# Optimization experiments

Hardware: AMD Instinct MI355X
Metric: run time of the kernel (lower is better)

## Reference

```python
import jax, jax.numpy as jnp
import numpy as np

S, B, D_IN = 2048, 32, 512
H, PROJ, L = 1024, 512, 2
LN_EPS = 1e-5


def setup_inputs() -> dict:
    key = jax.random.key(0)
    ks = jax.random.split(key, 4)
    X = jax.random.normal(ks[0], (S, B, D_IN), dtype=jnp.float32)
    W = jax.random.normal(ks[1], (L, 3 * H, D_IN), dtype=jnp.float32) * (1.0 / np.sqrt(D_IN))
    b = jax.random.normal(ks[2], (L, 3 * H), dtype=jnp.float32) * 0.01
    P = jax.random.normal(ks[3], (L, PROJ, H), dtype=jnp.float32) * (1.0 / np.sqrt(H))
    gamma = jnp.ones((L, PROJ), dtype=jnp.float32)
    beta = jnp.zeros((L, PROJ), dtype=jnp.float32)
    return {"X": X, "W": W, "b": b, "P": P, "gamma": gamma, "beta": beta}


def _forget_mult(F, Z):
    # h_t = f_t * z_t + (1 - f_t) * h_{t-1}, h_0 = 0  (ForgetMult, hidden=None)
    def step(c, fz):
        f, z = fz
        c = f * z + (1.0 - f) * c
        return c, c
    c0 = jnp.zeros_like(Z[0])
    _, C = jax.lax.scan(step, c0, (F, Z))
    return C  # (S, B, H)


def _layer_norm(x, g, be):
    mu = jnp.mean(x, axis=-1, keepdims=True)
    var = jnp.mean(jnp.square(x - mu), axis=-1, keepdims=True)
    return (x - mu) * jax.lax.rsqrt(var + LN_EPS) * g + be


def reference(X, W, b, P, gamma, beta):
    inp = X
    last_states = []
    for i in range(L):
        # linear: (S,B,in) @ (in,3H) + b  -> gates
        Y = jnp.einsum('sbd,gd->sbg', inp, W[i]) + b[i]
        Z, F, O = jnp.split(Y, 3, axis=-1)
        Z = jnp.tanh(Z)
        F = jax.nn.sigmoid(F)
        C = _forget_mult(F, Z)                      # (S,B,H)
        Hout = jax.nn.sigmoid(O) * C                # output gate (QRNN-fo)
        inp = jnp.einsum('sbh,ph->sbp', Hout, P[i])  # projection, no bias
        inp = _layer_norm(inp, gamma[i], beta[i])
        last_states.append(C[-1])                   # (B,H)
    next_hidden = jnp.stack(last_states, axis=0)     # (L,B,H)
    return inp, next_hidden
```

## Files before the change

### kernel.cpp

```cpp
#include <hip/hip_runtime.h>
#include <hip/hip_bf16.h>

typedef _Float16 f16x8 __attribute__((ext_vector_type(8)));
typedef _Float16 f16x4 __attribute__((ext_vector_type(4)));
typedef float f32x4 __attribute__((ext_vector_type(4)));

#define SEQ 2048
#define BATCH 32
#define DIN 512
#define HID 1024
#define PROJ 512
#define ROWS (SEQ*BATCH)
#define G3H (3*HID)

#define AS1(p) ((const __attribute__((address_space(1))) void*)(p))
#define AS3(p) ((__attribute__((address_space(3))) void*)(p))

__global__ __launch_bounds__(256)
void cvt_f32_f16(const float* __restrict__ in, _Float16* __restrict__ out, int n4)
{
    int i = blockIdx.x * 256 + threadIdx.x;
    if (i >= n4) return;
    float4 v = ((const float4*)in)[i];
    f16x4 o;
    o[0] = (_Float16)v.x; o[1] = (_Float16)v.y;
    o[2] = (_Float16)v.z; o[3] = (_Float16)v.w;
    ((f16x4*)out)[i] = o;
}

template<int MODE>
__global__ __launch_bounds__(256)
void gemm_lds(const _Float16* __restrict__ A, const _Float16* __restrict__ Bm,
              const float* __restrict__ bias, _Float16* __restrict__ C,
              int N, int K, int HH)
{
    __shared__ __align__(16) _Float16 sA[128][32];
    __shared__ __align__(16) _Float16 sB[128][32];

    const int tid  = threadIdx.x;
    const int lane = tid & 63;
    const int wave = tid >> 6;
    const int wm = wave >> 1;
    const int wn = wave & 1;
    const size_t row0 = (size_t)blockIdx.y * 128;
    const size_t col0 = (size_t)blockIdx.x * 128;

    const int crow = lane >> 2;
    const int ccol = (lane & 3) * 8;

    f32x4 acc[4][4] = {};

    const int rl = lane & 15;
    const int kb = (lane >> 4) * 8;

    const int nk = K / 32;
    for (int kt = 0; kt < nk; ++kt) {
#pragma unroll
        for (int c2 = 0; c2 < 2; ++c2) {
            const int c = wave * 2 + c2;
            const _Float16* ga = A  + (row0 + c * 16 + crow) * (size_t)K + kt * 32 + ccol;
            const _Float16* gb = Bm + (col0 + c * 16 + crow) * (size_t)K + kt * 32 + ccol;
            __builtin_amdgcn_global_load_lds(AS1(ga), AS3(&sA[c * 16][0]), 16, 0, 0);
            __builtin_amdgcn_global_load_lds(AS1(gb), AS3(&sB[c * 16][0]), 16, 0, 0);
        }
        __syncthreads();

        f16x8 af[4], bf[4];
#pragma unroll
        for (int m = 0; m < 4; ++m)
            af[m] = *(const f16x8*)&sA[wm * 64 + m * 16 + rl][kb];
#pragma unroll
        for (int n = 0; n < 4; ++n)
            bf[n] = *(const f16x8*)&sB[wn * 64 + n * 16 + rl][kb];
#pragma unroll
        for (int m = 0; m < 4; ++m)
#pragma unroll
            for (int n = 0; n < 4; ++n)
                acc[m][n] = __builtin_amdgcn_mfma_f32_16x16x32_f16(af[m], bf[n], acc[m][n], 0, 0, 0);
        __syncthreads();
    }

#pragma unroll
    for (int m = 0; m < 4; ++m) {
#pragma unroll
        for (int n = 0; n < 4; ++n) {
            const size_t col = col0 + wn * 64 + n * 16 + rl;
            const size_t row = row0 + wm * 64 + m * 16 + (lane >> 4) * 4;
            float bv = (MODE == 0) ? bias[col] : 0.f;
#pragma unroll
            for (int j = 0; j < 4; ++j) {
                float v = acc[m][n][j];
                if (MODE == 0) {
                    v += bv;
                    if ((int)col < HH) {
                        float vc = fminf(fmaxf(v, -15.f), 15.f);
                        float e = __expf(2.f * vc);
                        v = (e - 1.f) / (e + 1.f);
                    } else {
                        v = 1.f / (1.f + __expf(-v));
                    }
                }
                C[(row + j) * (size_t)N + col] = (_Float16)v;
            }
        }
    }
}

__global__ __launch_bounds__(64)
void scan_kernel(const _Float16* __restrict__ Y, _Float16* __restrict__ Ho,
                 float* __restrict__ carry, float* __restrict__ hid,
                 int nS, int first)
{
    const int t = blockIdx.x * 64 + threadIdx.x;
    const int h = t & (HID - 1);
    const int b = t >> 10;
    const _Float16* pz = Y + (size_t)b * G3H + h;
    _Float16* po = Ho + (size_t)b * HID + h;
    const size_t strideY = (size_t)BATCH * G3H;
    const size_t strideH = (size_t)BATCH * HID;
    float c = first ? 0.f : carry[t];
#pragma unroll 8
    for (int s = 0; s < nS; ++s) {
        float z = (float)pz[(size_t)s * strideY];
        float f = (float)pz[(size_t)s * strideY + HID];
        float o = (float)pz[(size_t)s * strideY + 2 * HID];
        c = f * z + (1.f - f) * c;
        po[(size_t)s * strideH] = (_Float16)(o * c);
    }
    carry[t] = c;
    if (hid) hid[t] = c;
}

template<int OUT32>
__global__ __launch_bounds__(256)
void ln_kernel(const _Float16* __restrict__ Xin, const float* __restrict__ g,
               const float* __restrict__ be, _Float16* __restrict__ o16,
               float* __restrict__ o32)
{
    const int row  = blockIdx.x * 4 + (threadIdx.x >> 6);
    const int lane = threadIdx.x & 63;
    const _Float16* p = Xin + (size_t)row * PROJ + lane * 8;
    f16x8 v = *(const f16x8*)p;
    float x[8];
    float s = 0.f;
#pragma unroll
    for (int j = 0; j < 8; ++j) { x[j] = (float)v[j]; s += x[j]; }
#pragma unroll
    for (int d = 1; d < 64; d <<= 1) s += __shfl_xor(s, d);
    const float mu = s * (1.f / PROJ);
    float s2 = 0.f;
#pragma unroll
    for (int j = 0; j < 8; ++j) { float dd = x[j] - mu; s2 += dd * dd; }
#pragma unroll
    for (int d = 1; d < 64; d <<= 1) s2 += __shfl_xor(s2, d);
    const float rstd = rsqrtf(s2 * (1.f / PROJ) + 1e-5f);

    float y[8];
#pragma unroll
    for (int j = 0; j < 8; ++j)
        y[j] = (x[j] - mu) * rstd * g[lane * 8 + j] + be[lane * 8 + j];

    if (OUT32) {
        float* q = o32 + (size_t)row * PROJ + lane * 8;
        ((float4*)q)[0] = make_float4(y[0], y[1], y[2], y[3]);
        ((float4*)q)[1] = make_float4(y[4], y[5], y[6], y[7]);
    } else {
        f16x8 o;
#pragma unroll
        for (int j = 0; j < 8; ++j) o[j] = (_Float16)y[j];
        *(f16x8*)(o16 + (size_t)row * PROJ + lane * 8) = o;
    }
}

extern "C" void kernel_launch(void* const* d_in, const int* in_sizes, int n_in,
                              void* d_out, int out_size, void* d_ws, size_t ws_size,
                              hipStream_t stream)
{
    const float* X     = (const float*)d_in[0];
    const float* W     = (const float*)d_in[1];
    const float* b     = (const float*)d_in[2];
    const float* P     = (const float*)d_in[3];
    const float* gamma = (const float*)d_in[4];
    const float* beta  = (const float*)d_in[5];
    float* out = (float*)d_out;

    char* w = (char*)d_ws;
    _Float16* Xh = (_Float16*)w; w += (size_t)ROWS * DIN * 2;
    _Float16* Wh = (_Float16*)w; w += (size_t)2 * G3H * DIN * 2;
    _Float16* Ph = (_Float16*)w; w += (size_t)2 * PROJ * HID * 2;
    float* carry = (float*)w;    w += (size_t)BATCH * HID * 4;
    const size_t fixed = (size_t)(w - (char*)d_ws);

    const int cands[7] = {2048, 1024, 512, 256, 128, 64, 32};
    int CS = 32;
    for (int i = 0; i < 7; ++i) {
        size_t need = fixed + (size_t)cands[i] * 32 * (G3H + HID + PROJ) * 2;
        if (need <= ws_size) { CS = cands[i]; break; }
    }
    _Float16* Yg = (_Float16*)w; w += (size_t)CS * 32 * G3H * 2;
    _Float16* Ho = (_Float16*)w; w += (size_t)CS * 32 * HID * 2;
    _Float16* G2 = (_Float16*)w;

    cvt_f32_f16<<<(ROWS * DIN / 4 + 255) / 256, 256, 0, stream>>>(X, Xh, ROWS * DIN / 4);
    cvt_f32_f16<<<(2 * G3H * DIN / 4 + 255) / 256, 256, 0, stream>>>(W, Wh, 2 * G3H * DIN / 4);
    cvt_f32_f16<<<(2 * PROJ * HID / 4 + 255) / 256, 256, 0, stream>>>(P, Ph, 2 * PROJ * HID / 4);

    float* hid = out + (size_t)ROWS * PROJ;
    const int nch = SEQ / CS;
    const int rows = CS * BATCH;

    for (int i = 0; i < 2; ++i) {
        for (int ch = 0; ch < nch; ++ch) {
            const size_t r0 = (size_t)ch * rows;
            gemm_lds<0><<<dim3(G3H / 128, rows / 128), 256, 0, stream>>>(
                Xh + r0 * DIN, Wh + (size_t)i * G3H * DIN, b + i * G3H, Yg, G3H, DIN, HID);
            scan_kernel<<<(BATCH * HID) / 64, 64, 0, stream>>>(
                Yg, Ho, carry, (ch == nch - 1) ? hid + (size_t)i * BATCH * HID : nullptr,
                CS, ch == 0);
            gemm_lds<1><<<dim3(PROJ / 128, rows / 128), 256, 0, stream>>>(
                Ho, Ph + (size_t)i * PROJ * HID, nullptr, G2, PROJ, HID, 0);
            if (i == 0)
                ln_kernel<0><<<rows / 4, 256, 0, stream>>>(G2, gamma, beta, Xh + r0 * PROJ, nullptr);
            else
                ln_kernel<1><<<rows / 4, 256, 0, stream>>>(G2, gamma + PROJ, beta + PROJ, nullptr, out + r0 * PROJ);
        }
    }
}
```

Before: 1.857 ms.

## Parallelize forget-mult scan over sequence segments and double-buffer GEMM LDS tiles

Replaces the single sequential scan over each chunk with a three-pass segmented scan: each of 16 segments computes its affine (A,B) composition, a middle pass chains segment carries, and a second pass recomputes outputs from the segment start states. This multiplies the number of threads working on the recurrence so the latency-bound scan can fill the GPU, at the cost of reading the Z/F gates twice and extra workspace. The GEMM also gains a two-stage LDS buffer that prefetches the next K tile while computing the current one, and uses fast division in the activation epilogue.

Result: faster. 1.590 ms (-14.4%).

```diff
diff --git a/kernel.cpp b/kernel.cpp
--- a/kernel.cpp
+++ b/kernel.cpp
@@ -12,6 +12,8 @@
 #define PROJ 512
 #define ROWS (SEQ*BATCH)
 #define G3H (3*HID)
+#define NSEG 16
+#define NCHAIN (BATCH*HID)
 
 #define AS1(p) ((const __attribute__((address_space(1))) void*)(p))
 #define AS3(p) ((__attribute__((address_space(3))) void*)(p))
@@ -34,8 +36,8 @@
               const float* __restrict__ bias, _Float16* __restrict__ C,
               int N, int K, int HH)
 {
-    __shared__ __align__(16) _Float16 sA[128][32];
-    __shared__ __align__(16) _Float16 sB[128][32];
+    __shared__ __align__(16) _Float16 sA[2][128][32];
+    __shared__ __align__(16) _Float16 sB[2][128][32];
 
     const int tid  = threadIdx.x;
     const int lane = tid & 63;
@@ -52,33 +54,48 @@
 
     const int rl = lane & 15;
     const int kb = (lane >> 4) * 8;
-
     const int nk = K / 32;
+
+    const int c0 = wave * 2, c1 = wave * 2 + 1;
+    const _Float16* gA0 = A  + (row0 + c0 * 16 + crow) * (size_t)K + ccol;
+    const _Float16* gA1 = A  + (row0 + c1 * 16 + crow) * (size_t)K + ccol;
+    const _Float16* gB0 = Bm + (col0 + c0 * 16 + crow) * (size_t)K + ccol;
+    const _Float16* gB1 = Bm + (col0 + c1 * 16 + crow) * (size_t)K + ccol;
+
+#define STAGE(buf, kt)                                                          \
+    do {                                                                        \
+        __builtin_amdgcn_global_load_lds(AS1(gA0 + (size_t)(kt) * 32),          \
+                                         AS3(&sA[buf][c0 * 16][0]), 16, 0, 0);  \
+        __builtin_amdgcn_global_load_lds(AS1(gB0 + (size_t)(kt) * 32),          \
+                                         AS3(&sB[buf][c0 * 16][0]), 16, 0, 0);  \
+        __builtin_amdgcn_global_load_lds(AS1(gA1 + (size_t)(kt) * 32),          \
+                                         AS3(&sA[buf][c1 * 16][0]), 16, 0, 0);  \
+        __builtin_amdgcn_global_load_lds(AS1(gB1 + (size_t)(kt) * 32),          \
+                                         AS3(&sB[buf][c1 * 16][0]), 16, 0, 0);  \
+    } while (0)
+
+    int cur = 0;
+    STAGE(0, 0);
+    __syncthreads();
+
     for (int kt = 0; kt < nk; ++kt) {
-#pragma unroll
-        for (int c2 = 0; c2 < 2; ++c2) {
-            const int c = wave * 2 + c2;
-            const _Float16* ga = A  + (row0 + c * 16 + crow) * (size_t)K + kt * 32 + ccol;
-            const _Float16* gb = Bm + (col0 + c * 16 + crow) * (size_t)K + kt * 32 + ccol;
-            __builtin_amdgcn_global_load_lds(AS1(ga), AS3(&sA[c * 16][0]), 16, 0, 0);
-            __builtin_amdgcn_global_load_lds(AS1(gb), AS3(&sB[c * 16][0]), 16, 0, 0);
-        }
-        __syncthreads();
-
+        if (kt + 1 < nk) STAGE(cur ^ 1, kt + 1);
         f16x8 af[4], bf[4];
 #pragma unroll
         for (int m = 0; m < 4; ++m)
-            af[m] = *(const f16x8*)&sA[wm * 64 + m * 16 + rl][kb];
+            af[m] = *(const f16x8*)&sA[cur][wm * 64 + m * 16 + rl][kb];
 #pragma unroll
         for (int n = 0; n < 4; ++n)
-            bf[n] = *(const f16x8*)&sB[wn * 64 + n * 16 + rl][kb];
+            bf[n] = *(const f16x8*)&sB[cur][wn * 64 + n * 16 + rl][kb];
 #pragma unroll
         for (int m = 0; m < 4; ++m)
 #pragma unroll
             for (int n = 0; n < 4; ++n)
                 acc[m][n] = __builtin_amdgcn_mfma_f32_16x16x32_f16(af[m], bf[n], acc[m][n], 0, 0, 0);
         __syncthreads();
-    }
+        cur ^= 1;
+    }
+#undef STAGE
 
 #pragma unroll
     for (int m = 0; m < 4; ++m) {
@@ -95,9 +112,9 @@
                     if ((int)col < HH) {
                         float vc = fminf(fmaxf(v, -15.f), 15.f);
                         float e = __expf(2.f * vc);
-                        v = (e - 1.f) / (e + 1.f);
+                        v = __fdividef(e - 1.f, e + 1.f);
                     } else {
-                        v = 1.f / (1.f + __expf(-v));
+                        v = __fdividef(1.f, 1.f + __expf(-v));
                     }
                 }
                 C[(row + j) * (size_t)N + col] = (_Float16)v;
@@ -106,29 +123,69 @@
     }
 }
 
-__global__ __launch_bounds__(64)
-void scan_kernel(const _Float16* __restrict__ Y, _Float16* __restrict__ Ho,
-                 float* __restrict__ carry, float* __restrict__ hid,
-                 int nS, int first)
-{
-    const int t = blockIdx.x * 64 + threadIdx.x;
+
+__global__ __launch_bounds__(256)
+void scan_p1(const _Float16* __restrict__ Y, float* __restrict__ Aseg,
+             float* __restrict__ Bseg, int SL)
+{
+    const int t = blockIdx.x * 256 + threadIdx.x;
+    const int g = blockIdx.y;
     const int h = t & (HID - 1);
     const int b = t >> 10;
-    const _Float16* pz = Y + (size_t)b * G3H + h;
-    _Float16* po = Ho + (size_t)b * HID + h;
+    const _Float16* pz = Y + ((size_t)(g * SL) * BATCH + b) * G3H + h;
+    const size_t strideY = (size_t)BATCH * G3H;
+    float A = 1.f, Bv = 0.f;
+#pragma unroll 4
+    for (int k = 0; k < SL; ++k) {
+        float z = (float)pz[0];
+        float f = (float)pz[HID];
+        Bv = f * z + (1.f - f) * Bv;
+        A *= (1.f - f);
+        pz += strideY;
+    }
+    Aseg[(size_t)g * NCHAIN + t] = A;
+    Bseg[(size_t)g * NCHAIN + t] = Bv;
+}
+
+__global__ __launch_bounds__(256)
+void scan_mid(const float* __restrict__ Aseg, const float* __restrict__ Bseg,
+              float* __restrict__ cst, float* __restrict__ carry,
+              float* __restrict__ hid, int first)
+{
+    const int t = blockIdx.x * 256 + threadIdx.x;
+    float c = first ? 0.f : carry[t];
+#pragma unroll
+    for (int g = 0; g < NSEG; ++g) {
+        cst[(size_t)g * NCHAIN + t] = c;
+        c = Bseg[(size_t)g * NCHAIN + t] + Aseg[(size_t)g * NCHAIN + t] * c;
+    }
+    carry[t] = c;
+    if (hid) hid[t] = c;
+}
+
+__global__ __launch_bounds__(256)
+void scan_p2(const _Float16* __restrict__ Y, const float* __restrict__ cst,
+             _Float16* __restrict__ Ho, int SL)
+{
+    const int t = blockIdx.x * 256 + threadIdx.x;
+    const int g = blockIdx.y;
+    const int h = t & (HID - 1);
+    const int b = t >> 10;
+    const _Float16* pz = Y + ((size_t)(g * SL) * BATCH + b) * G3H + h;
+    _Float16* po = Ho + ((size_t)(g * SL) * BATCH + b) * HID + h;
     const size_t strideY = (size_t)BATCH * G3H;
     const size_t strideH = (size_t)BATCH * HID;
-    float c = first ? 0.f : carry[t];
-#pragma unroll 8
-    for (int s = 0; s < nS; ++s) {
-        float z = (float)pz[(size_t)s * strideY];
-        float f = (float)pz[(size_t)s * strideY + HID];
-        float o = (float)pz[(size_t)s * strideY + 2 * HID];
+    float c = cst[(size_t)g * NCHAIN + t];
+#pragma unroll 4
+    for (int k = 0; k < SL; ++k) {
+        float z = (float)pz[0];
+        float f = (float)pz[HID];
+        float o = (float)pz[2 * HID];
         c = f * z + (1.f - f) * c;
-        po[(size_t)s * strideH] = (_Float16)(o * c);
-    }
-    carry[t] = c;
-    if (hid) hid[t] = c;
+        *po = (_Float16)(o * c);
+        pz += strideY;
+        po += strideH;
+    }
 }
 
 template<int OUT32>
@@ -188,7 +245,10 @@
     _Float16* Xh = (_Float16*)w; w += (size_t)ROWS * DIN * 2;
     _Float16* Wh = (_Float16*)w; w += (size_t)2 * G3H * DIN * 2;
     _Float16* Ph = (_Float16*)w; w += (size_t)2 * PROJ * HID * 2;
-    float* carry = (float*)w;    w += (size_t)BATCH * HID * 4;
+    float* carry = (float*)w;    w += (size_t)NCHAIN * 4;
+    float* Aseg  = (float*)w;    w += (size_t)NSEG * NCHAIN * 4;
+    float* Bseg  = (float*)w;    w += (size_t)NSEG * NCHAIN * 4;
+    float* cst   = (float*)w;    w += (size_t)NSEG * NCHAIN * 4;
     const size_t fixed = (size_t)(w - (char*)d_ws);
 
     const int cands[7] = {2048, 1024, 512, 256, 128, 64, 32};
@@ -208,15 +268,18 @@
     float* hid = out + (size_t)ROWS * PROJ;
     const int nch = SEQ / CS;
     const int rows = CS * BATCH;
+    const int SL = CS / NSEG;
 
     for (int i = 0; i < 2; ++i) {
         for (int ch = 0; ch < nch; ++ch) {
             const size_t r0 = (size_t)ch * rows;
             gemm_lds<0><<<dim3(G3H / 128, rows / 128), 256, 0, stream>>>(
                 Xh + r0 * DIN, Wh + (size_t)i * G3H * DIN, b + i * G3H, Yg, G3H, DIN, HID);
-            scan_kernel<<<(BATCH * HID) / 64, 64, 0, stream>>>(
-                Yg, Ho, carry, (ch == nch - 1) ? hid + (size_t)i * BATCH * HID : nullptr,
-                CS, ch == 0);
+            scan_p1<<<dim3(NCHAIN / 256, NSEG), 256, 0, stream>>>(Yg, Aseg, Bseg, SL);
+            scan_mid<<<NCHAIN / 256, 256, 0, stream>>>(
+                Aseg, Bseg, cst, carry,
+                (ch == nch - 1) ? hid + (size_t)i * NCHAIN : nullptr, ch == 0);
+            scan_p2<<<dim3(NCHAIN / 256, NSEG), 256, 0, stream>>>(Yg, cst, Ho, SL);
             gemm_lds<1><<<dim3(PROJ / 128, rows / 128), 256, 0, stream>>>(
                 Ho, Ph + (size_t)i * PROJ * HID, nullptr, G2, PROJ, HID, 0);
             if (i == 0)
```
